# Optimization experiments

Hardware: AMD Instinct MI355X
Metric: run time of the kernel (lower is better)

The kernel has to match this reference:

```python
import jax, jax.numpy as jnp
import numpy as np

WS, NH = 7, 12  # window_size, num_heads
DIM, B, H, W = 384, 32, 56, 56


def _rel_index(ws):
    coords = np.stack(np.meshgrid(np.arange(ws), np.arange(ws), indexing='ij')).reshape(2, -1)
    rel = (coords[:, :, None] - coords[:, None, :]).transpose(1, 2, 0)
    rel[..., 0] += ws - 1
    rel[..., 1] += ws - 1
    rel[..., 0] *= 2 * ws - 1
    return jnp.asarray(rel.sum(-1), dtype=jnp.int32)  # [ws*ws, ws*ws]


def setup_inputs() -> dict:
    key = jax.random.key(0)
    k1, k2, k3, k4, k5 = jax.random.split(key, 5)
    x = jax.random.normal(k1, (B, DIM, H, W), dtype=jnp.float32)
    w_qkv = jax.random.normal(k2, (3 * DIM, DIM), dtype=jnp.float32) * (DIM ** -0.5)
    w_proj = jax.random.normal(k3, (DIM, DIM), dtype=jnp.float32) * (DIM ** -0.5)
    b_proj = jax.random.normal(k4, (DIM,), dtype=jnp.float32) * 0.02
    bias_table = jax.random.normal(k5, ((2 * WS - 1) ** 2, NH), dtype=jnp.float32) * 0.02
    rel_index = _rel_index(WS)
    return {"x": x, "w_qkv": w_qkv, "w_proj": w_proj, "b_proj": b_proj,
            "bias_table": bias_table, "rel_index": rel_index}


def reference(x, w_qkv, w_proj, b_proj, bias_table, rel_index):
    b, c, h, w = x.shape
    hd = c // NH
    scale = hd ** -0.5
    hh, ww = h // WS, w // WS
    # 1x1 conv == channel matmul
    qkv = jnp.einsum('bchw,oc->bohw', x, w_qkv)  # [b, 3c, h, w]
    qkv = qkv.reshape(b, 3, NH, hd, hh, WS, ww, WS)
    # -> [3, b*hh*ww, nh, ws*ws, hd]
    qkv = qkv.transpose(1, 0, 4, 6, 2, 5, 7, 3).reshape(3, b * hh * ww, NH, WS * WS, hd)
    q, k, v = qkv[0], qkv[1], qkv[2]
    bias = bias_table[rel_index].transpose(2, 0, 1)  # [nh, ws*ws, ws*ws]
    dots = jnp.einsum('wnid,wnjd->wnij', q, k) * scale + bias[None]
    attn = jax.nn.softmax(dots, axis=-1)
    out = jnp.einsum('wnij,wnjd->wnid', attn, v)
    # back to [b, c, h, w]
    out = out.reshape(b, hh, ww, NH, WS, WS, hd).transpose(0, 3, 6, 1, 4, 2, 5).reshape(b, c, h, w)
    out = jnp.einsum('bchw,oc->bohw', out, w_proj) + b_proj[None, :, None, None]
    return out
```

## Files before the change

### kernel.cpp

```cpp
#include <hip/hip_runtime.h>

#define NH 12
#define HD 32
#define DIMC 384
#define BATCH 32
#define HWIMG 56
#define NWIN 2048
#define NROWS 100352
#define QKV_M 1152
#define KDIM 384
#define QSCALE 0.17677669529663687f

typedef __attribute__((ext_vector_type(8))) short short8;
typedef __attribute__((ext_vector_type(4))) short short4v;
typedef __attribute__((ext_vector_type(4))) float f32x4;

typedef const __attribute__((address_space(1))) unsigned int* gas_ptr;
typedef __attribute__((address_space(3))) unsigned int* las_ptr;

__device__ __forceinline__ unsigned short f2bf(float f) {
    union { float f; unsigned u; } v; v.f = f;
    unsigned r = v.u + 0x7FFF + ((v.u >> 16) & 1);
    return (unsigned short)(r >> 16);
}

__global__ __launch_bounds__(256) void cvt_w(const float* __restrict__ in,
                                             unsigned short* __restrict__ out, int n) {
    int i = blockIdx.x * 256 + threadIdx.x;
    if (i < n) out[i] = f2bf(in[i]);
}

__global__ __launch_bounds__(256) void cvt_x(const float* __restrict__ x,
                                             unsigned short* __restrict__ xt) {
    __shared__ float tile[32][33];
    const int b = blockIdx.z, c0 = blockIdx.y * 32, n0 = blockIdx.x * 32;
    const int tid = threadIdx.x;
    const int cl = tid >> 5, nl = tid & 31;
    #pragma unroll
    for (int p = 0; p < 4; ++p)
        tile[cl + p * 8][nl] = x[((size_t)b * DIMC + c0 + cl + p * 8) * 3136 + n0 + nl];
    __syncthreads();
    const int nl2 = tid >> 3, cq = (tid & 7) * 4;
    const int n = n0 + nl2;
    const int nh = n / HWIMG, nw = n % HWIMG;
    const int row = ((b * 64 + (nh / 7) * 8 + nw / 7) * 49 + (nh % 7) * 7 + nw % 7);
    short4v pk;
    #pragma unroll
    for (int u = 0; u < 4; ++u) pk[u] = (short)f2bf(tile[cq + u][nl2]);
    *(short4v*)(xt + (size_t)row * KDIM + c0 + cq) = pk;
}

__global__ __launch_bounds__(256) void fill_bias(const float* __restrict__ bias_table,
                                                 const int* __restrict__ rel_index,
                                                 float* __restrict__ biasp) {
    int id = blockIdx.x * 256 + threadIdx.x;
    int h = id >> 12, r = id & 4095;
    int j = r >> 6, i = r & 63;
    float v = 0.f;
    if (i < 49 && j < 49) v = bias_table[rel_index[i * 49 + j] * NH + h];
    biasp[id] = v;
}

__global__ __launch_bounds__(256) void gemm_qkv(
    const unsigned short* __restrict__ A,
    const unsigned short* __restrict__ Bm,
    unsigned short* __restrict__ qk)
{
    __shared__ char LBUF[32768];
    char* Al = LBUF;
    char* Bl = LBUF + 16384;
    const int tid = threadIdx.x;

    constexpr int MT = 9;
    const unsigned nwg = gridDim.x;
    const unsigned lin = blockIdx.x;
    const unsigned swz = (lin & 7) * (nwg >> 3) + (lin >> 3);
    const int m0 = (int)(swz % MT) * 128;
    const int ng0 = (int)(swz / MT) * 128;

    const int lane = tid & 63;
    const int wv = tid >> 6;
    const int wr = wv >> 1, wc = wv & 1;
    const int lrow = lane & 15, kgrp = lane >> 4;

    f32x4 acc[4][4] = {};

    const char* Abase = (const char*)(A + (size_t)m0 * KDIM);
    const char* Bbase = (const char*)(Bm + (size_t)ng0 * KDIM);

    for (int kt = 0; kt < KDIM / 64; ++kt) {
        const int kb = kt * 128;
        #pragma unroll
        for (int it = 0; it < 4; ++it) {
            int chunk = it * 256 + tid;
            int row = chunk >> 3, slot = chunk & 7;
            int scol = (slot ^ (row & 7)) * 16;
            __builtin_amdgcn_global_load_lds(
                (gas_ptr)(Abase + (size_t)row * (KDIM * 2) + kb + scol),
                (las_ptr)(Al + chunk * 16), 16, 0, 0);
        }
        #pragma unroll
        for (int it = 0; it < 4; ++it) {
            int chunk = it * 256 + tid;
            int row = chunk >> 3, slot = chunk & 7;
            int scol = (slot ^ (row & 7)) * 16;
            __builtin_amdgcn_global_load_lds(
                (gas_ptr)(Bbase + (size_t)row * (KDIM * 2) + kb + scol),
                (las_ptr)(Bl + chunk * 16), 16, 0, 0);
        }
        __syncthreads();
        #pragma unroll
        for (int kk = 0; kk < 2; ++kk) {
            short8 af[4], bfr[4];
            #pragma unroll
            for (int i = 0; i < 4; ++i) {
                int row = wr * 64 + i * 16 + lrow;
                int slot = (kk * 4 + kgrp) ^ (row & 7);
                af[i] = *(const short8*)(Al + row * 128 + slot * 16);
            }
            #pragma unroll
            for (int j = 0; j < 4; ++j) {
                int row = wc * 64 + j * 16 + lrow;
                int slot = (kk * 4 + kgrp) ^ (row & 7);
                bfr[j] = *(const short8*)(Bl + row * 128 + slot * 16);
            }
            __builtin_amdgcn_s_setprio(1);
            #pragma unroll
            for (int i = 0; i < 4; ++i)
                #pragma unroll
                for (int j = 0; j < 4; ++j)
                    acc[i][j] = __builtin_amdgcn_mfma_f32_16x16x32_bf16(af[i], bfr[j], acc[i][j], 0, 0, 0);
            __builtin_amdgcn_s_setprio(0);
        }
        __syncthreads();
    }

    const float sc = (m0 < 384) ? QSCALE : 1.0f;
    #pragma unroll
    for (int i = 0; i < 4; ++i) {
        int mpl = wr * 64 + i * 16 + kgrp * 4;
        #pragma unroll
        for (int j = 0; j < 4; ++j) {
            int ngl = wc * 64 + j * 16 + lrow;
            short4v pk;
            pk.x = (short)f2bf(acc[i][j].x * sc);
            pk.y = (short)f2bf(acc[i][j].y * sc);
            pk.z = (short)f2bf(acc[i][j].z * sc);
            pk.w = (short)f2bf(acc[i][j].w * sc);
            *(short4v*)(LBUF + ngl * 256 + ((mpl * 2) ^ ((ngl & 7) << 4))) = pk;
        }
    }
    __syncthreads();
    #pragma unroll
    for (int p = 0; p < 8; ++p) {
        int ch = p * 256 + tid;
        int ngl = ch >> 4, q = ch & 15;
        short8 v = *(const short8*)(LBUF + ngl * 256 + ((q * 16) ^ ((ngl & 7) << 4)));
        *(short8*)(qk + (size_t)(ng0 + ngl) * QKV_M + m0 + q * 8) = v;
    }
}

__global__ __launch_bounds__(256) void gemm_proj(
    const unsigned short* __restrict__ A,
    const unsigned short* __restrict__ Bm,
    const float* __restrict__ bias,
    float* __restrict__ C)
{
    __shared__ char Al[128 * 128];
    __shared__ char Bl[128 * 128];
    const int tid = threadIdx.x;

    constexpr int MT = 3;
    const unsigned nwg = gridDim.x;
    const unsigned lin = blockIdx.x;
    const unsigned swz = (lin & 7) * (nwg >> 3) + (lin >> 3);
    const int m0 = (int)(swz % MT) * 128;
    const int ng0 = (int)(swz / MT) * 128;

    const int lane = tid & 63;
    const int wv = tid >> 6;
    const int wr = wv >> 1, wc = wv & 1;
    const int lrow = lane & 15, kgrp = lane >> 4;

    f32x4 acc[4][4] = {};

    const char* Abase = (const char*)(A + (size_t)m0 * KDIM);
    const char* Bbase = (const char*)(Bm + (size_t)ng0 * KDIM);

    for (int kt = 0; kt < KDIM / 64; ++kt) {
        const int kb = kt * 128;
        #pragma unroll
        for (int it = 0; it < 4; ++it) {
            int chunk = it * 256 + tid;
            int row = chunk >> 3, slot = chunk & 7;
            int scol = (slot ^ (row & 7)) * 16;
            __builtin_amdgcn_global_load_lds(
                (gas_ptr)(Abase + (size_t)row * (KDIM * 2) + kb + scol),
                (las_ptr)(Al + chunk * 16), 16, 0, 0);
        }
        #pragma unroll
        for (int it = 0; it < 4; ++it) {
            int chunk = it * 256 + tid;
            int row = chunk >> 3, slot = chunk & 7;
            int scol = (slot ^ (row & 7)) * 16;
            __builtin_amdgcn_global_load_lds(
                (gas_ptr)(Bbase + (size_t)row * (KDIM * 2) + kb + scol),
                (las_ptr)(Bl + chunk * 16), 16, 0, 0);
        }
        __syncthreads();
        #pragma unroll
        for (int kk = 0; kk < 2; ++kk) {
            short8 af[4], bfr[4];
            #pragma unroll
            for (int i = 0; i < 4; ++i) {
                int row = wr * 64 + i * 16 + lrow;
                int slot = (kk * 4 + kgrp) ^ (row & 7);
                af[i] = *(const short8*)(Al + row * 128 + slot * 16);
            }
            #pragma unroll
            for (int j = 0; j < 4; ++j) {
                int row = wc * 64 + j * 16 + lrow;
                int slot = (kk * 4 + kgrp) ^ (row & 7);
                bfr[j] = *(const short8*)(Bl + row * 128 + slot * 16);
            }
            __builtin_amdgcn_s_setprio(1);
            #pragma unroll
            for (int i = 0; i < 4; ++i)
                #pragma unroll
                for (int j = 0; j < 4; ++j)
                    acc[i][j] = __builtin_amdgcn_mfma_f32_16x16x32_bf16(af[i], bfr[j], acc[i][j], 0, 0, 0);
            __builtin_amdgcn_s_setprio(0);
        }
        __syncthreads();
    }

    #pragma unroll
    for (int i = 0; i < 4; ++i) {
        int m = m0 + wr * 64 + i * 16 + kgrp * 4;
        float b0 = bias[m + 0], b1 = bias[m + 1], b2 = bias[m + 2], b3 = bias[m + 3];
        #pragma unroll
        for (int j = 0; j < 4; ++j) {
            int ng = ng0 + wc * 64 + j * 16 + lrow;
            unsigned bb = (unsigned)ng / 3136u;
            unsigned nsp = (unsigned)ng - bb * 3136u;
            C[((size_t)bb * DIMC + m + 0) * 3136 + nsp] = acc[i][j].x + b0;
            C[((size_t)bb * DIMC + m + 1) * 3136 + nsp] = acc[i][j].y + b1;
            C[((size_t)bb * DIMC + m + 2) * 3136 + nsp] = acc[i][j].z + b2;
            C[((size_t)bb * DIMC + m + 3) * 3136 + nsp] = acc[i][j].w + b3;
        }
    }
}

__global__ __launch_bounds__(256) void win_attn(
    const unsigned short* __restrict__ qkw,
    const float* __restrict__ biasp,
    unsigned short* __restrict__ att)
{
    __shared__ short Vl[4][32 * 72];
    const int tid = threadIdx.x;
    const int lane = tid & 63;
    const int wv = tid >> 6;
    const int g = lane >> 4, c = lane & 15;
    const int bid = blockIdx.x;
    const int swz = (bid & 7) * 768 + (bid >> 3);
    const int W = swz * 4 + wv;
    const int win = W / 12;
    const int head = W - win * 12;

    short* Vw = Vl[wv];

    #pragma unroll
    for (int u = 0; u < 8; ++u) {
        int id = u * 64 + lane;
        if (id < 480) {
            int d = id / 15, jj = 49 + id % 15;
            Vw[d * 72 + jj] = 0;
        }
    }

    const unsigned short* qbase = qkw + (size_t)win * 49 * QKV_M + head * HD;

    short8 kf[4], qf[4];
    #pragma unroll
    for (int a = 0; a < 4; ++a) {
        int r = a * 16 + c; if (r > 48) r = 48;
        qf[a] = *(const short8*)(qbase + (size_t)r * QKV_M + g * 8);
        kf[a] = *(const short8*)(qbase + (size_t)r * QKV_M + DIMC + g * 8);
    }

    const unsigned short* vsrc = qbase + 2 * DIMC;
    #pragma unroll
    for (int p = 0; p < 4; ++p) {
        int r = p * 16 + (lane >> 2);
        int chk = (lane & 3) * 8;
        if (r < 49) {
            short8 v8 = *(const short8*)(vsrc + (size_t)r * QKV_M + chk);
            #pragma unroll
            for (int u = 0; u < 8; ++u)
                Vw[(chk + u) * 72 + r] = v8[u];
        }
    }

    f32x4 s[4][4] = {};
    #pragma unroll
    for (int a = 0; a < 4; ++a)
        #pragma unroll
        for (int bi = 0; bi < 4; ++bi)
            s[a][bi] = __builtin_amdgcn_mfma_f32_16x16x32_bf16(kf[a], qf[bi], s[a][bi], 0, 0, 0);

    const float* bp = biasp + head * 4096;
    #pragma unroll
    for (int bi = 0; bi < 4; ++bi) {
        float mx = -1e30f;
        #pragma unroll
        for (int a = 0; a < 4; ++a) {
            #pragma unroll
            for (int e = 0; e < 4; ++e) {
                int j = a * 16 + g * 4 + e;
                float sv = s[a][bi][e] + bp[j * 64 + bi * 16 + c];
                sv = (j < 49) ? sv : -1e30f;
                s[a][bi][e] = sv;
                mx = fmaxf(mx, sv);
            }
        }
        mx = fmaxf(mx, __shfl_xor(mx, 16));
        mx = fmaxf(mx, __shfl_xor(mx, 32));
        float sum = 0.f;
        #pragma unroll
        for (int a = 0; a < 4; ++a) {
            #pragma unroll
            for (int e = 0; e < 4; ++e) {
                int j = a * 16 + g * 4 + e;
                float pv = (j < 49) ? __expf(s[a][bi][e] - mx) : 0.f;
                s[a][bi][e] = pv;
                sum += pv;
            }
        }
        sum += __shfl_xor(sum, 16);
        sum += __shfl_xor(sum, 32);
        float inv = 1.0f / sum;
        #pragma unroll
        for (int a = 0; a < 4; ++a)
            #pragma unroll
            for (int e = 0; e < 4; ++e)
                s[a][bi][e] *= inv;
    }

    unsigned pk[4][4][2];
    #pragma unroll
    for (int a = 0; a < 4; ++a)
        #pragma unroll
        for (int bi = 0; bi < 4; ++bi)
            #pragma unroll
            for (int h = 0; h < 2; ++h)
                pk[a][bi][h] = (unsigned)f2bf(s[a][bi][2 * h]) |
                               ((unsigned)f2bf(s[a][bi][2 * h + 1]) << 16);

    short8 vf[2][2];
    #pragma unroll
    for (int tn = 0; tn < 2; ++tn)
        #pragma unroll
        for (int ks = 0; ks < 2; ++ks)
            vf[tn][ks] = *(const short8*)(&Vw[(tn * 16 + c) * 72 + ks * 32 + g * 8]);

    f32x4 o[4][2] = {};
    const int gsel = g >> 1;
    const int sgb = 2 * (g & 1);
    #pragma unroll
    for (int ks = 0; ks < 2; ++ks) {
        #pragma unroll
        for (int to = 0; to < 4; ++to) {
            union { int w[4]; short8 v; } u;
            #pragma unroll
            for (int w = 0; w < 4; ++w) {
                int srcl = ((sgb + (w >> 1)) * 16 + c) << 2;
                int rA = __builtin_amdgcn_ds_bpermute(srcl, (int)pk[ks * 2 + 0][to][w & 1]);
                int rB = __builtin_amdgcn_ds_bpermute(srcl, (int)pk[ks * 2 + 1][to][w & 1]);
                u.w[w] = gsel ? rB : rA;
            }
            #pragma unroll
            for (int tn = 0; tn < 2; ++tn)
                o[to][tn] = __builtin_amdgcn_mfma_f32_16x16x32_bf16(u.v, vf[tn][ks], o[to][tn], 0, 0, 0);
        }
    }

    const int wl = win & 63, bb = win >> 6;
    const size_t obase = (size_t)bb * 3136 * DIMC;
    const int nsp0 = (wl >> 3) * 7 * HWIMG + (wl & 7) * 7;
    #pragma unroll
    for (int to = 0; to < 4; ++to) {
        #pragma unroll
        for (int e = 0; e < 4; ++e) {
            int i = to * 16 + g * 4 + e;
            if (i < 49) {
                int nsp = nsp0 + (i / 7) * HWIMG + (i % 7);
                unsigned short* ob = att + obase + (size_t)nsp * DIMC + head * HD;
                #pragma unroll
                for (int tn = 0; tn < 2; ++tn)
                    ob[tn * 16 + c] = f2bf(o[to][tn][e]);
            }
        }
    }
}

extern "C" void kernel_launch(void* const* d_in, const int* in_sizes, int n_in,
                              void* d_out, int out_size, void* d_ws, size_t ws_size,
                              hipStream_t stream) {
    const float* x          = (const float*)d_in[0];
    const float* w_qkv      = (const float*)d_in[1];
    const float* w_proj     = (const float*)d_in[2];
    const float* b_proj     = (const float*)d_in[3];
    const float* bias_table = (const float*)d_in[4];
    const int*   rel_index  = (const int*)d_in[5];

    unsigned short* xt    = (unsigned short*)d_ws;
    unsigned short* att   = xt;
    unsigned short* qkw2  = xt + (size_t)NROWS * KDIM;
    unsigned short* wqb   = qkw2 + (size_t)NROWS * QKV_M;
    unsigned short* wpb   = wqb + QKV_M * KDIM;
    float*          biasp = (float*)(wpb + DIMC * KDIM);

    cvt_w<<<(QKV_M * KDIM + 255) / 256, 256, 0, stream>>>(w_qkv, wqb, QKV_M * KDIM);
    cvt_w<<<(DIMC * KDIM + 255) / 256, 256, 0, stream>>>(w_proj, wpb, DIMC * KDIM);
    cvt_x<<<dim3(98, 12, BATCH), 256, 0, stream>>>(x, xt);
    fill_bias<<<192, 256, 0, stream>>>(bias_table, rel_index, biasp);

    gemm_qkv<<<7056, 256, 0, stream>>>(wqb, xt, qkw2);

    win_attn<<<6144, 256, 0, stream>>>(qkw2, biasp, att);

    gemm_proj<<<2352, 256, 0, stream>>>(wpb, att, b_proj, (float*)d_out);
}
```

Baseline: 323.6 us.

## Stage attention output per window in LDS for coalesced stores; fold Q scale into weights

```diff
diff --git a/kernel.cpp b/kernel.cpp
--- a/kernel.cpp
+++ b/kernel.cpp
@@ -25,9 +25,14 @@
 }
 
 __global__ __launch_bounds__(256) void cvt_w(const float* __restrict__ in,
-                                             unsigned short* __restrict__ out, int n) {
+                                             unsigned short* __restrict__ out,
+                                             int n, int scale_elems) {
     int i = blockIdx.x * 256 + threadIdx.x;
-    if (i < n) out[i] = f2bf(in[i]);
+    if (i < n) {
+        float v = in[i];
+        if (i < scale_elems) v *= QSCALE;
+        out[i] = f2bf(v);
+    }
 }
 
 __global__ __launch_bounds__(256) void cvt_x(const float* __restrict__ x,
@@ -135,7 +140,6 @@
         __syncthreads();
     }
 
-    const float sc = (m0 < 384) ? QSCALE : 1.0f;
     #pragma unroll
     for (int i = 0; i < 4; ++i) {
         int mpl = wr * 64 + i * 16 + kgrp * 4;
@@ -143,10 +147,10 @@
         for (int j = 0; j < 4; ++j) {
             int ngl = wc * 64 + j * 16 + lrow;
             short4v pk;
-            pk.x = (short)f2bf(acc[i][j].x * sc);
-            pk.y = (short)f2bf(acc[i][j].y * sc);
-            pk.z = (short)f2bf(acc[i][j].z * sc);
-            pk.w = (short)f2bf(acc[i][j].w * sc);
+            pk.x = (short)f2bf(acc[i][j].x);
+            pk.y = (short)f2bf(acc[i][j].y);
+            pk.z = (short)f2bf(acc[i][j].z);
+            pk.w = (short)f2bf(acc[i][j].w);
             *(short4v*)(LBUF + ngl * 256 + ((mpl * 2) ^ ((ngl & 7) << 4))) = pk;
         }
     }
@@ -251,23 +255,21 @@
     }
 }
 
-__global__ __launch_bounds__(256) void win_attn(
+__global__ __launch_bounds__(768) void win_attn(
     const unsigned short* __restrict__ qkw,
     const float* __restrict__ biasp,
     unsigned short* __restrict__ att)
 {
-    __shared__ short Vl[4][32 * 72];
+    __shared__ short SM[12 * 2304];
     const int tid = threadIdx.x;
     const int lane = tid & 63;
     const int wv = tid >> 6;
     const int g = lane >> 4, c = lane & 15;
     const int bid = blockIdx.x;
-    const int swz = (bid & 7) * 768 + (bid >> 3);
-    const int W = swz * 4 + wv;
-    const int win = W / 12;
-    const int head = W - win * 12;
-
-    short* Vw = Vl[wv];
+    const int win = (bid & 7) * 256 + (bid >> 3);
+    const int head = wv;
+
+    short* Vw = SM + wv * 2304;
 
     #pragma unroll
     for (int u = 0; u < 8; ++u) {
@@ -384,21 +386,33 @@
         }
     }
 
+    __syncthreads();
+    short* Ol = SM;
+    #pragma unroll
+    for (int to = 0; to < 4; ++to) {
+        #pragma unroll
+        for (int e = 0; e < 4; ++e) {
+            int i = to * 16 + g * 4 + e;
+            if (i < 49) {
+                #pragma unroll
+                for (int tn = 0; tn < 2; ++tn)
+                    Ol[i * 392 + head * HD + tn * 16 + c] = (short)f2bf(o[to][tn][e]);
+            }
+        }
+    }
+    __syncthreads();
+
     const int wl = win & 63, bb = win >> 6;
     const size_t obase = (size_t)bb * 3136 * DIMC;
     const int nsp0 = (wl >> 3) * 7 * HWIMG + (wl & 7) * 7;
     #pragma unroll
-    for (int to = 0; to < 4; ++to) {
-        #pragma unroll
-        for (int e = 0; e < 4; ++e) {
-            int i = to * 16 + g * 4 + e;
-            if (i < 49) {
-                int nsp = nsp0 + (i / 7) * HWIMG + (i % 7);
-                unsigned short* ob = att + obase + (size_t)nsp * DIMC + head * HD;
-                #pragma unroll
-                for (int tn = 0; tn < 2; ++tn)
-                    ob[tn * 16 + c] = f2bf(o[to][tn][e]);
-            }
+    for (int p = 0; p < 4; ++p) {
+        int ch = p * 768 + tid;
+        if (ch < 2352) {
+            int row = ch / 48, q = ch - row * 48;
+            int nsp = nsp0 + (row / 7) * HWIMG + row % 7;
+            short8 v = *(const short8*)(Ol + row * 392 + q * 8);
+            *(short8*)(att + obase + (size_t)nsp * DIMC + q * 8) = v;
         }
     }
 }
@@ -420,14 +434,14 @@
     unsigned short* wpb   = wqb + QKV_M * KDIM;
     float*          biasp = (float*)(wpb + DIMC * KDIM);
 
-    cvt_w<<<(QKV_M * KDIM + 255) / 256, 256, 0, stream>>>(w_qkv, wqb, QKV_M * KDIM);
-    cvt_w<<<(DIMC * KDIM + 255) / 256, 256, 0, stream>>>(w_proj, wpb, DIMC * KDIM);
+    cvt_w<<<(QKV_M * KDIM + 255) / 256, 256, 0, stream>>>(w_qkv, wqb, QKV_M * KDIM, DIMC * KDIM);
+    cvt_w<<<(DIMC * KDIM + 255) / 256, 256, 0, stream>>>(w_proj, wpb, DIMC * KDIM, 0);
     cvt_x<<<dim3(98, 12, BATCH), 256, 0, stream>>>(x, xt);
     fill_bias<<<192, 256, 0, stream>>>(bias_table, rel_index, biasp);
 
     gemm_qkv<<<7056, 256, 0, stream>>>(wqb, xt, qkw2);
 
-    win_attn<<<6144, 256, 0, stream>>>(qkw2, biasp, att);
+    win_attn<<<2048, 768, 0, stream>>>(qkw2, biasp, att);
 
     gemm_proj<<<2352, 256, 0, stream>>>(wpb, att, b_proj, (float*)d_out);
 }
```

Result: slower. 349.6 us (+8.0%).
